# Kernel tuning notes

Hardware: AMD Instinct MI355X
Metric: run time of the kernel (lower is better)

## Reference

```python
import jax, jax.numpy as jnp
import numpy as np
from math import sqrt

H = 16  # head_num


def setup_inputs() -> dict:
    key = jax.random.key(0)
    ks = jax.random.split(key, 8)
    B, Sq, Skv, Dq, Dkv, Dall = 2, 2048, 2048, 1024, 1024, 1024
    x = jax.random.normal(ks[0], (B, Sq, Dq), dtype=jnp.float32)
    y = jax.random.normal(ks[1], (B, Skv, Dkv), dtype=jnp.float32)
    attention_mask = jnp.ones((B, 1, Sq, Skv), dtype=jnp.int32)
    # torch nn.Linear weights are [out, in]
    Wq = jax.random.normal(ks[2], (Dall, Dq), dtype=jnp.float32) * 0.02
    Wk = jax.random.normal(ks[3], (Dall, Dkv), dtype=jnp.float32) * 0.02
    Wv = jax.random.normal(ks[4], (Dall, Dkv), dtype=jnp.float32) * 0.02
    Wo = jax.random.normal(ks[5], (Dq, Dall), dtype=jnp.float32) * 0.02
    bo = jnp.zeros((Dq,), dtype=jnp.float32)
    return {"x": x, "y": y, "attention_mask": attention_mask,
            "Wq": Wq, "Wk": Wk, "Wv": Wv, "Wo": Wo, "bo": bo}


def reference(x, y, attention_mask, Wq, Wk, Wv, Wo, bo):
    B, Sq, _ = x.shape
    Dall = Wq.shape[0]
    Dh = Dall // H
    # projections (torch Linear: x @ W.T), split heads -> [B, H, S, Dh]
    q = (x @ Wq.T).reshape(B, Sq, H, Dh).transpose(0, 2, 1, 3)
    k = (y @ Wk.T).reshape(B, -1, H, Dh).transpose(0, 2, 1, 3)
    v = (y @ Wv.T).reshape(B, -1, H, Dh).transpose(0, 2, 1, 3)
    scores = jnp.einsum('bhqd,bhkd->bhqk', q, k)  # [B,H,Sq,Skv]
    mask = (attention_mask == 0)  # masked_fill where mask.eq(0) -> but torch does mask.eq(0) then fills True positions
    scores = jnp.where(mask, jnp.float32(-1e9), scores)
    # NOTE: faithful quirk - mask applied before scaling; scale uses sqrt(h_size)
    attn = jax.nn.softmax(scores / sqrt(Dh), axis=-1)
    out = jnp.einsum('bhqk,bhkd->bhqd', attn, v)
    out = out.transpose(0, 2, 1, 3).reshape(B, Sq, Dall)
    return out @ Wo.T + bo
```

## Files before the change

### kernel.cpp

```cpp
#include <hip/hip_runtime.h>
#include <stdint.h>


typedef __attribute__((ext_vector_type(8))) short bf16x8;
typedef __attribute__((ext_vector_type(4))) float f32x4;
typedef __attribute__((ext_vector_type(16))) float f32x16;
typedef __attribute__((ext_vector_type(2))) unsigned int u32x2;

#define LOG2E 1.44269504088896f
#define QSCALE (0.125f * LOG2E)

static __device__ __forceinline__ unsigned short f2bf(float f) {
  union { float f; unsigned int u; } v; v.f = f;
  unsigned int r = v.u + 0x7FFFu + ((v.u >> 16) & 1u);
  return (unsigned short)(r >> 16);
}

static __device__ __forceinline__ void g2l16(const void* gsrc, void* ldst) {
  __builtin_amdgcn_global_load_lds((const __attribute__((address_space(1))) unsigned int*)gsrc,
                                   (__attribute__((address_space(3))) unsigned int*)ldst,
                                   16, 0, 0);
}

static __device__ __forceinline__ unsigned int cvt_pk_bf16(float lo, float hi) {
  unsigned int r;
  asm("v_cvt_pk_bf16_f32 %0, %1, %2" : "=v"(r) : "v"(lo), "v"(hi));
  return r;
}

static __device__ __forceinline__ u32x2 pl32swap(unsigned int a, unsigned int b) {
  return __builtin_amdgcn_permlane32_swap(a, b, false, false);
}

static __device__ __forceinline__ f32x16 mfma32(bf16x8 a, bf16x8 b, f32x16 c) {
  return __builtin_amdgcn_mfma_f32_32x32x16_bf16(a, b, c, 0, 0, 0);
}

static __device__ __forceinline__ size_t kfrag_addr(int row, int col) {
  int b = row >> 11, s = row & 2047;
  int h = col >> 6, d = col & 63;
  int t32 = s >> 5, r31 = s & 31;
  int ks = d >> 4, r5 = (d >> 3) & 1, e = d & 7;
  return (size_t)(b * 16 + h) * 131072 + (size_t)t32 * 2048 + ks * 512 + (r5 * 32 + r31) * 8 + e;
}
static __device__ __forceinline__ size_t vfrag_addr(int row, int col) {
  int b = row >> 11, s = row & 2047;
  int h = col >> 6, d = col & 63;
  int t64 = s >> 6, k2 = (s >> 4) & 3, r5 = (s >> 3) & 1, e = s & 7;
  int mb = d >> 5, r31 = d & 31;
  return (size_t)(b * 16 + h) * 131072 + (size_t)t64 * 4096 + (mb * 4 + k2) * 512 + (r5 * 32 + r31) * 8 + e;
}

__global__ void k_prep(const float* __restrict__ x, const float* __restrict__ y,
                       const float* __restrict__ Wq, const float* __restrict__ Wk,
                       const float* __restrict__ Wv, const float* __restrict__ Wo,
                       const int* __restrict__ mask,
                       unsigned short* __restrict__ xb, unsigned short* __restrict__ yb,
                       unsigned short* __restrict__ Wqb, unsigned short* __restrict__ Wkb,
                       unsigned short* __restrict__ Wvb, unsigned short* __restrict__ Wob,
                       unsigned long long* __restrict__ bits, unsigned int* __restrict__ flag) {
  const int task = blockIdx.y;
  if (task == 6) {
    const int lane = threadIdx.x & 63;
    int gw = blockIdx.x * 4 + (threadIdx.x >> 6);
    bool any0 = false;
    for (; gw < 131072; gw += 4096) {
      int m = mask[(size_t)gw * 64 + lane];
      unsigned long long bal = __ballot(m != 0);
      if (lane == 0) {
        bits[gw] = bal;
        any0 |= (bal != ~0ull);
      }
    }
    if (lane == 0 && any0) atomicAnd(flag, 0u);
    return;
  }
  const float* in; unsigned short* out; int n;
  switch (task) {
    case 0: in = x;  out = xb;  n = 4194304; break;
    case 1: in = y;  out = yb;  n = 4194304; break;
    case 2: in = Wq; out = Wqb; n = 1048576; break;
    case 3: in = Wk; out = Wkb; n = 1048576; break;
    case 4: in = Wv; out = Wvb; n = 1048576; break;
    default: in = Wo; out = Wob; n = 1048576; break;
  }
  int i = (blockIdx.x * blockDim.x + threadIdx.x) * 4;
  const int stride = gridDim.x * blockDim.x * 4;
  for (; i < n; i += stride) {
    float4 v = *reinterpret_cast<const float4*>(in + i);
    ushort4 o;
    o.x = f2bf(v.x); o.y = f2bf(v.y); o.z = f2bf(v.z); o.w = f2bf(v.w);
    *reinterpret_cast<ushort4*>(out + i) = o;
  }
}

template <int OM>
static __device__ __forceinline__ void gemm_body(const unsigned short* __restrict__ A,
                                                 const unsigned short* __restrict__ W,
                                                 void* __restrict__ Cout,
                                                 float scale) {
  __shared__ __align__(16) unsigned short As[128 * 32];
  __shared__ __align__(16) unsigned short Bs[128 * 32];
  const int tid = threadIdx.x;
  const int w = tid >> 6, lane = tid & 63;
  const int wr = w >> 1, wc = w & 1;
  const int l15 = lane & 15, lg = lane >> 4;
  const int bm = blockIdx.x, bn = blockIdx.y;

  f32x4 acc[4][4] = {};

  const int e0 = w * 1024 + lane * 8;
  const int e1 = e0 + 512;
  const int r0 = e0 >> 5, c0 = e0 & 31;
  const int r1 = e1 >> 5, c1 = e1 & 31;
  const unsigned short* A0 = A + (size_t)(bm * 128 + r0) * 1024 + c0;
  const unsigned short* A1 = A + (size_t)(bm * 128 + r1) * 1024 + c1;
  const unsigned short* W0 = W + (size_t)(bn * 128 + r0) * 1024 + c0;
  const unsigned short* W1 = W + (size_t)(bn * 128 + r1) * 1024 + c1;

  for (int kt = 0; kt < 1024; kt += 32) {
    g2l16(A0 + kt, (char*)As + e0 * 2);
    g2l16(A1 + kt, (char*)As + e1 * 2);
    g2l16(W0 + kt, (char*)Bs + e0 * 2);
    g2l16(W1 + kt, (char*)Bs + e1 * 2);
    __syncthreads();
    bf16x8 a[4], b[4];
#pragma unroll
    for (int mi = 0; mi < 4; ++mi)
      a[mi] = *reinterpret_cast<const bf16x8*>(As + (wr * 64 + mi * 16 + l15) * 32 + lg * 8);
#pragma unroll
    for (int ni = 0; ni < 4; ++ni)
      b[ni] = *reinterpret_cast<const bf16x8*>(Bs + (wc * 64 + ni * 16 + l15) * 32 + lg * 8);
#pragma unroll
    for (int mi = 0; mi < 4; ++mi)
#pragma unroll
      for (int ni = 0; ni < 4; ++ni)
        acc[mi][ni] = __builtin_amdgcn_mfma_f32_16x16x32_bf16(a[mi], b[ni], acc[mi][ni], 0, 0, 0);
    __syncthreads();
  }

#pragma unroll
  for (int ni = 0; ni < 4; ++ni) {
    const int gcol = bn * 128 + wc * 64 + ni * 16 + l15;
#pragma unroll
    for (int mi = 0; mi < 4; ++mi) {
#pragma unroll
      for (int r = 0; r < 4; ++r) {
        const int grow = bm * 128 + wr * 64 + mi * 16 + lg * 4 + r;
        if (OM == 2)
          ((unsigned short*)Cout)[kfrag_addr(grow, gcol)] = f2bf(acc[mi][ni][r] * scale);
        else
          ((unsigned short*)Cout)[vfrag_addr(grow, gcol)] = f2bf(acc[mi][ni][r]);
      }
    }
  }
}

__global__ __launch_bounds__(256) void k_gemm_qkv(
    const unsigned short* __restrict__ xb, const unsigned short* __restrict__ yb,
    const unsigned short* __restrict__ Wq, const unsigned short* __restrict__ Wk,
    const unsigned short* __restrict__ Wv,
    unsigned short* __restrict__ Qf, unsigned short* __restrict__ Kf,
    unsigned short* __restrict__ Vf) {
  const int z = blockIdx.z;
  if (z == 0) gemm_body<2>(xb, Wq, Qf, QSCALE);
  else if (z == 1) gemm_body<2>(yb, Wk, Kf, 1.f);
  else gemm_body<3>(yb, Wv, Vf, 1.f);
}

__global__ __launch_bounds__(256) void k_gemm_o(
    const unsigned short* __restrict__ A, const unsigned short* __restrict__ W,
    float* __restrict__ out, const float* __restrict__ bo) {
  __shared__ __align__(16) unsigned short As[64 * 32];
  __shared__ __align__(16) unsigned short Bs[128 * 32];
  const int tid = threadIdx.x;
  const int w = tid >> 6, lane = tid & 63;
  const int l15 = lane & 15, lg = lane >> 4;
  const int bm = blockIdx.x, bn = blockIdx.y;

  f32x4 acc[4][2] = {};

  const int ea = tid * 8;
  const int eb0 = tid * 8;
  const int eb1 = eb0 + 2048;
  const int ra = ea >> 5, ca = ea & 31;
  const int rb0 = eb0 >> 5, cb0 = eb0 & 31;
  const int rb1 = eb1 >> 5, cb1 = eb1 & 31;
  const unsigned short* A0 = A + (size_t)(bm * 64 + ra) * 1024 + ca;
  const unsigned short* W0 = W + (size_t)(bn * 128 + rb0) * 1024 + cb0;
  const unsigned short* W1 = W + (size_t)(bn * 128 + rb1) * 1024 + cb1;

  for (int kt = 0; kt < 1024; kt += 32) {
    g2l16(A0 + kt, (char*)As + ea * 2);
    g2l16(W0 + kt, (char*)Bs + eb0 * 2);
    g2l16(W1 + kt, (char*)Bs + eb1 * 2);
    __syncthreads();
    bf16x8 a[4], b[2];
#pragma unroll
    for (int mi = 0; mi < 4; ++mi)
      a[mi] = *reinterpret_cast<const bf16x8*>(As + (mi * 16 + l15) * 32 + lg * 8);
#pragma unroll
    for (int ni = 0; ni < 2; ++ni)
      b[ni] = *reinterpret_cast<const bf16x8*>(Bs + (w * 32 + ni * 16 + l15) * 32 + lg * 8);
#pragma unroll
    for (int mi = 0; mi < 4; ++mi)
#pragma unroll
      for (int ni = 0; ni < 2; ++ni)
        acc[mi][ni] = __builtin_amdgcn_mfma_f32_16x16x32_bf16(a[mi], b[ni], acc[mi][ni], 0, 0, 0);
    __syncthreads();
  }

#pragma unroll
  for (int ni = 0; ni < 2; ++ni) {
    const int gcol = bn * 128 + w * 32 + ni * 16 + l15;
    const float bv = bo[gcol];
#pragma unroll
    for (int mi = 0; mi < 4; ++mi) {
#pragma unroll
      for (int r = 0; r < 4; ++r) {
        const int grow = bm * 64 + mi * 16 + lg * 4 + r;
        out[(size_t)grow * 1024 + gcol] = acc[mi][ni][r] + bv;
      }
    }
  }
}


#define BUILD_PB2(SP, K2, IDX) {                                   \
    unsigned int c0_ = cvt_pk_bf16(SP[(K2)*8 + 0], SP[(K2)*8 + 1]);\
    unsigned int c1_ = cvt_pk_bf16(SP[(K2)*8 + 2], SP[(K2)*8 + 3]);\
    unsigned int c2_ = cvt_pk_bf16(SP[(K2)*8 + 4], SP[(K2)*8 + 5]);\
    unsigned int c3_ = cvt_pk_bf16(SP[(K2)*8 + 6], SP[(K2)*8 + 7]);\
    u32x2 r0_ = pl32swap(c0_, c2_);                                \
    u32x2 r1_ = pl32swap(c1_, c3_);                                \
    union { unsigned int u[4]; bf16x8 v; } f_;                     \
    f_.u[0] = r0_.x; f_.u[1] = r1_.x; f_.u[2] = r0_.y; f_.u[3] = r1_.y; \
    pb[IDX] = f_.v; }

#define STAGE128(T, BUF) {                                                    \
    const char* ks_ = Kg + (size_t)(T) * 16384;                               \
    const char* vs_ = Vg + (size_t)(T) * 16384;                               \
    char* db_ = smem + (BUF) * 32768;                                         \
    const int lo_ = tid * 16;                                                 \
    _Pragma("unroll")                                                         \
    for (int c_ = 0; c_ < 4; ++c_) {                                          \
      g2l16(ks_ + c_ * 4096 + lo_, db_ + c_ * 4096 + lo_);                    \
      g2l16(vs_ + c_ * 4096 + lo_, db_ + 16384 + c_ * 4096 + lo_);            \
    }                                                                         \
  }

#define HALF_BODY(BASE, HALF, TW)                                             \
  {                                                                           \
    const char* Kb = (BASE) + (HALF) * 8192;                                  \
    const char* Vb = (BASE) + 16384 + (HALF) * 8192;                          \
    bf16x8 kf[8], vf[8];                                                      \
    _Pragma("unroll")                                                         \
    for (int f = 0; f < 8; ++f)                                               \
      kf[f] = *reinterpret_cast<const bf16x8*>(Kb + f * 1024 + lane * 16);    \
    f32x16 s0 = z16, s1 = z16;                                                \
    __builtin_amdgcn_s_setprio(1);                                            \
    _Pragma("unroll")                                                         \
    for (int ks = 0; ks < 4; ++ks) {                                          \
      s0 = mfma32(kf[ks], qf[ks], s0);                                        \
      s1 = mfma32(kf[4 + ks], qf[ks], s1);                                    \
    }                                                                         \
    __builtin_amdgcn_s_setprio(0);                                            \
    _Pragma("unroll")                                                         \
    for (int f = 0; f < 8; ++f)                                               \
      vf[f] = *reinterpret_cast<const bf16x8*>(Vb + f * 1024 + lane * 16);    \
    if (!allfull) {                                                           \
      unsigned long long wb = brow[TW];                                       \
      if (!__all(wb == ~0ull)) {                                              \
        _Pragma("unroll")                                                     \
        for (int r = 0; r < 16; ++r) {                                        \
          const int kl = (r & 3) + 8 * (r >> 2) + 4 * hi;                     \
          s0[r] = ((wb >> kl) & 1ull) ? s0[r] : -1e9f;                        \
          s1[r] = ((wb >> (kl + 32)) & 1ull) ? s1[r] : -1e9f;                 \
        }                                                                     \
      }                                                                       \
    }                                                                         \
    _Pragma("unroll")                                                         \
    for (int r = 0; r < 16; ++r) {                                            \
      s0[r] = __builtin_amdgcn_exp2f(s0[r]);                                  \
      s1[r] = __builtin_amdgcn_exp2f(s1[r]);                                  \
    }                                                                         \
    {                                                                         \
      float sm[8];                                                            \
      _Pragma("unroll")                                                       \
      for (int r = 0; r < 8; ++r) sm[r] = (s0[r] + s0[r + 8]) + (s1[r] + s1[r + 8]); \
      sm[0] += sm[4]; sm[1] += sm[5]; sm[2] += sm[6]; sm[3] += sm[7];         \
      sm[0] += sm[2]; sm[1] += sm[3];                                         \
      float ls = sm[0] + sm[1];                                               \
      u32x2 sw = pl32swap(__builtin_bit_cast(unsigned int, ls),               \
                          __builtin_bit_cast(unsigned int, ls));              \
      l_run += __builtin_bit_cast(float, sw.x) + __builtin_bit_cast(float, sw.y); \
    }                                                                         \
    bf16x8 pb[4];                                                             \
    BUILD_PB2(s0, 0, 0) BUILD_PB2(s0, 1, 1) BUILD_PB2(s1, 0, 2) BUILD_PB2(s1, 1, 3) \
    __builtin_amdgcn_s_setprio(1);                                            \
    _Pragma("unroll")                                                         \
    for (int k2 = 0; k2 < 4; ++k2) {                                          \
      o0 = mfma32(vf[k2], pb[k2], o0);                                        \
      o1 = mfma32(vf[4 + k2], pb[k2], o1);                                    \
    }                                                                         \
    __builtin_amdgcn_s_setprio(0);                                            \
  }

__global__ __launch_bounds__(256, 2) void k_attn(
    const unsigned short* __restrict__ Qf, const unsigned short* __restrict__ Kf,
    const unsigned short* __restrict__ Vf, const unsigned long long* __restrict__ bits,
    const unsigned int* __restrict__ flag, unsigned short* __restrict__ AO) {
  __shared__ __align__(16) char smem[65536];
  const int tid = threadIdx.x, w = tid >> 6, lane = tid & 63;
  const int l31 = lane & 31, hi = lane >> 5;
  const int bid = blockIdx.x;
  const int xcd = bid & 7, rr = bid >> 3;
  const int j = rr & 15;
  const int g = xcd + ((rr >> 4) << 3);
  const int h = g & 15, b = g >> 4;
  const int q = j * 128 + w * 32 + l31;
  const bool allfull = (*flag == 0xFFFFFFFFu);
  const f32x16 z16 = {};

  const size_t bh = (size_t)(b * 16 + h) * 131072;
  bf16x8 qf[4];
  const unsigned short* Qp = Qf + bh + (size_t)(j * 4 + w) * 2048 + lane * 8;
#pragma unroll
  for (int ks = 0; ks < 4; ++ks)
    qf[ks] = *reinterpret_cast<const bf16x8*>(Qp + ks * 512);

  const char* Kg = (const char*)(Kf + bh);
  const char* Vg = (const char*)(Vf + bh);
  const unsigned long long* brow = bits + (size_t)(b * 2048 + q) * 32;

  f32x16 o0 = {}, o1 = {};
  float l_run = 0.f;

  STAGE128(0, 0)
  __syncthreads();

  for (int t = 0; t < 16; ++t) {
    const int cur = t & 1;
    if (t < 15) STAGE128(t + 1, cur ^ 1)
    const char* base = smem + cur * 32768;
    HALF_BODY(base, 0, 2 * t)
    HALF_BODY(base, 1, 2 * t + 1)
    __syncthreads();
  }

  const float inv = 1.f / l_run;
  unsigned short* Orow = AO + (size_t)(b * 2048 + q) * 1024 + h * 64;
#pragma unroll
  for (int g2 = 0; g2 < 4; ++g2) {
    ushort4 pk;
    pk.x = f2bf(o0[g2 * 4 + 0] * inv);
    pk.y = f2bf(o0[g2 * 4 + 1] * inv);
    pk.z = f2bf(o0[g2 * 4 + 2] * inv);
    pk.w = f2bf(o0[g2 * 4 + 3] * inv);
    *reinterpret_cast<ushort4*>(Orow + 8 * g2 + 4 * hi) = pk;
    pk.x = f2bf(o1[g2 * 4 + 0] * inv);
    pk.y = f2bf(o1[g2 * 4 + 1] * inv);
    pk.z = f2bf(o1[g2 * 4 + 2] * inv);
    pk.w = f2bf(o1[g2 * 4 + 3] * inv);
    *reinterpret_cast<ushort4*>(Orow + 32 + 8 * g2 + 4 * hi) = pk;
  }
}

extern "C" void kernel_launch(void* const* d_in, const int* in_sizes, int n_in,
                              void* d_out, int out_size, void* d_ws, size_t ws_size,
                              hipStream_t stream) {
  const float* x  = (const float*)d_in[0];
  const float* y  = (const float*)d_in[1];
  const int* mask = (const int*)d_in[2];
  const float* Wq = (const float*)d_in[3];
  const float* Wk = (const float*)d_in[4];
  const float* Wv = (const float*)d_in[5];
  const float* Wo = (const float*)d_in[6];
  const float* bo = (const float*)d_in[7];

  char* ws = (char*)d_ws;
  const size_t MB = 1ull << 20;
  unsigned short* xb  = (unsigned short*)(ws + 0 * MB);
  unsigned short* yb  = (unsigned short*)(ws + 8 * MB);
  unsigned short* Wqb = (unsigned short*)(ws + 16 * MB);
  unsigned short* Wkb = (unsigned short*)(ws + 18 * MB);
  unsigned short* Wvb = (unsigned short*)(ws + 20 * MB);
  unsigned short* Wob = (unsigned short*)(ws + 22 * MB);
  unsigned short* Qf  = (unsigned short*)(ws + 24 * MB);
  unsigned short* Kf  = (unsigned short*)(ws + 32 * MB);
  unsigned short* Vf  = (unsigned short*)(ws + 40 * MB);
  unsigned short* AOb = (unsigned short*)(ws + 56 * MB);
  unsigned long long* bits = (unsigned long long*)(ws + 64 * MB);
  unsigned int* flag = (unsigned int*)(ws + 65 * MB);

  hipMemsetAsync(flag, 0xFF, 4, stream);
  k_prep<<<dim3(1024, 7), 256, 0, stream>>>(x, y, Wq, Wk, Wv, Wo, mask,
                                            xb, yb, Wqb, Wkb, Wvb, Wob, bits, flag);
  k_gemm_qkv<<<dim3(32, 8, 3), 256, 0, stream>>>(xb, yb, Wqb, Wkb, Wvb, Qf, Kf, Vf);
  k_attn<<<512, 256, 0, stream>>>(Qf, Kf, Vf, bits, flag, AOb);
  k_gemm_o<<<dim3(64, 8), 256, 0, stream>>>(AOb, Wob, (float*)d_out, bo);
}
```

Before: 129.4 us.

## Software-pipeline attention loop: overlap next tile QK^T with current softmax/PV

Restructures the attention main loop from 16 iterations of 128-key tiles (two halves each) into 32 iterations of 64-key tiles. Each step computes the QK^T MFMAs for the next tile while softmax and PV run on the previous tile's scores and V fragments held in registers. LDS use is halved to 32KB of double buffers, with a sync per 64-key tile. The goal is to overlap exp and VALU work with MFMA, at the cost of more live registers (two score sets and two V fragment sets) and twice as many barriers. The s_setprio hints are also removed.

```diff
diff --git a/kernel.cpp b/kernel.cpp
--- a/kernel.cpp
+++ b/kernel.cpp
@@ -237,57 +237,39 @@
     f_.u[0] = r0_.x; f_.u[1] = r1_.x; f_.u[2] = r0_.y; f_.u[3] = r1_.y; \
     pb[IDX] = f_.v; }
 
-#define STAGE128(T, BUF) {                                                    \
-    const char* ks_ = Kg + (size_t)(T) * 16384;                               \
-    const char* vs_ = Vg + (size_t)(T) * 16384;                               \
-    char* db_ = smem + (BUF) * 32768;                                         \
-    const int lo_ = tid * 16;                                                 \
-    _Pragma("unroll")                                                         \
-    for (int c_ = 0; c_ < 4; ++c_) {                                          \
-      g2l16(ks_ + c_ * 4096 + lo_, db_ + c_ * 4096 + lo_);                    \
-      g2l16(vs_ + c_ * 4096 + lo_, db_ + 16384 + c_ * 4096 + lo_);            \
-    }                                                                         \
-  }
-
-#define HALF_BODY(BASE, HALF, TW)                                             \
+#define STAGE_TILE(T, BUF) {                                                  \
+    const size_t toff_ = (size_t)(T) * 8192;                                  \
+    char* kb_ = smem + (BUF) * 16384;                                         \
+    const int o0_ = (w * 2 + 0) * 1024 + lane * 16;                           \
+    const int o1_ = (w * 2 + 1) * 1024 + lane * 16;                           \
+    g2l16(Kg + toff_ + o0_, kb_ + o0_);                                       \
+    g2l16(Kg + toff_ + o1_, kb_ + o1_);                                       \
+    g2l16(Vg + toff_ + o0_, kb_ + 8192 + o0_);                                \
+    g2l16(Vg + toff_ + o1_, kb_ + 8192 + o1_);                                \
+  }
+
+#define SM_PV(S0, S1, VF, T)                                                  \
   {                                                                           \
-    const char* Kb = (BASE) + (HALF) * 8192;                                  \
-    const char* Vb = (BASE) + 16384 + (HALF) * 8192;                          \
-    bf16x8 kf[8], vf[8];                                                      \
-    _Pragma("unroll")                                                         \
-    for (int f = 0; f < 8; ++f)                                               \
-      kf[f] = *reinterpret_cast<const bf16x8*>(Kb + f * 1024 + lane * 16);    \
-    f32x16 s0 = z16, s1 = z16;                                                \
-    __builtin_amdgcn_s_setprio(1);                                            \
-    _Pragma("unroll")                                                         \
-    for (int ks = 0; ks < 4; ++ks) {                                          \
-      s0 = mfma32(kf[ks], qf[ks], s0);                                        \
-      s1 = mfma32(kf[4 + ks], qf[ks], s1);                                    \
-    }                                                                         \
-    __builtin_amdgcn_s_setprio(0);                                            \
-    _Pragma("unroll")                                                         \
-    for (int f = 0; f < 8; ++f)                                               \
-      vf[f] = *reinterpret_cast<const bf16x8*>(Vb + f * 1024 + lane * 16);    \
     if (!allfull) {                                                           \
-      unsigned long long wb = brow[TW];                                       \
+      unsigned long long wb = brow[T];                                        \
       if (!__all(wb == ~0ull)) {                                              \
         _Pragma("unroll")                                                     \
         for (int r = 0; r < 16; ++r) {                                        \
           const int kl = (r & 3) + 8 * (r >> 2) + 4 * hi;                     \
-          s0[r] = ((wb >> kl) & 1ull) ? s0[r] : -1e9f;                        \
-          s1[r] = ((wb >> (kl + 32)) & 1ull) ? s1[r] : -1e9f;                 \
+          S0[r] = ((wb >> kl) & 1ull) ? S0[r] : -1e9f;                        \
+          S1[r] = ((wb >> (kl + 32)) & 1ull) ? S1[r] : -1e9f;                 \
         }                                                                     \
       }                                                                       \
     }                                                                         \
     _Pragma("unroll")                                                         \
     for (int r = 0; r < 16; ++r) {                                            \
-      s0[r] = __builtin_amdgcn_exp2f(s0[r]);                                  \
-      s1[r] = __builtin_amdgcn_exp2f(s1[r]);                                  \
+      S0[r] = __builtin_amdgcn_exp2f(S0[r]);                                  \
+      S1[r] = __builtin_amdgcn_exp2f(S1[r]);                                  \
     }                                                                         \
     {                                                                         \
       float sm[8];                                                            \
       _Pragma("unroll")                                                       \
-      for (int r = 0; r < 8; ++r) sm[r] = (s0[r] + s0[r + 8]) + (s1[r] + s1[r + 8]); \
+      for (int r = 0; r < 8; ++r) sm[r] = (S0[r] + S0[r + 8]) + (S1[r] + S1[r + 8]); \
       sm[0] += sm[4]; sm[1] += sm[5]; sm[2] += sm[6]; sm[3] += sm[7];         \
       sm[0] += sm[2]; sm[1] += sm[3];                                         \
       float ls = sm[0] + sm[1];                                               \
@@ -296,21 +278,40 @@
       l_run += __builtin_bit_cast(float, sw.x) + __builtin_bit_cast(float, sw.y); \
     }                                                                         \
     bf16x8 pb[4];                                                             \
-    BUILD_PB2(s0, 0, 0) BUILD_PB2(s0, 1, 1) BUILD_PB2(s1, 0, 2) BUILD_PB2(s1, 1, 3) \
-    __builtin_amdgcn_s_setprio(1);                                            \
+    BUILD_PB2(S0, 0, 0) BUILD_PB2(S0, 1, 1) BUILD_PB2(S1, 0, 2) BUILD_PB2(S1, 1, 3) \
     _Pragma("unroll")                                                         \
     for (int k2 = 0; k2 < 4; ++k2) {                                          \
-      o0 = mfma32(vf[k2], pb[k2], o0);                                        \
-      o1 = mfma32(vf[4 + k2], pb[k2], o1);                                    \
+      o0 = mfma32(VF[k2], pb[k2], o0);                                        \
+      o1 = mfma32(VF[4 + k2], pb[k2], o1);                                    \
     }                                                                         \
-    __builtin_amdgcn_s_setprio(0);                                            \
+  }
+
+#define PIPE_STEP(sO0, sO1, vfO, sN0, sN1, vfN, T)                            \
+  {                                                                           \
+    const char* base_ = smem + (((T) + 1) & 1) * 16384;                       \
+    bf16x8 kf[8];                                                             \
+    _Pragma("unroll")                                                         \
+    for (int f = 0; f < 8; ++f)                                               \
+      kf[f] = *reinterpret_cast<const bf16x8*>(base_ + f * 1024 + lane * 16); \
+    sN0 = z16; sN1 = z16;                                                     \
+    _Pragma("unroll")                                                         \
+    for (int ks = 0; ks < 4; ++ks) {                                          \
+      sN0 = mfma32(kf[ks], qf[ks], sN0);                                      \
+      sN1 = mfma32(kf[4 + ks], qf[ks], sN1);                                  \
+    }                                                                         \
+    SM_PV(sO0, sO1, vfO, T)                                                   \
+    _Pragma("unroll")                                                         \
+    for (int f = 0; f < 8; ++f)                                               \
+      vfN[f] = *reinterpret_cast<const bf16x8*>(base_ + 8192 + f * 1024 + lane * 16); \
+    if ((T) <= 29) STAGE_TILE((T) + 2, (T) & 1)                               \
+    __syncthreads();                                                          \
   }
 
 __global__ __launch_bounds__(256, 2) void k_attn(
     const unsigned short* __restrict__ Qf, const unsigned short* __restrict__ Kf,
     const unsigned short* __restrict__ Vf, const unsigned long long* __restrict__ bits,
     const unsigned int* __restrict__ flag, unsigned short* __restrict__ AO) {
-  __shared__ __align__(16) char smem[65536];
+  __shared__ __align__(16) char smem[32768];
   const int tid = threadIdx.x, w = tid >> 6, lane = tid & 63;
   const int l31 = lane & 31, hi = lane >> 5;
   const int bid = blockIdx.x;
@@ -336,17 +337,35 @@
   f32x16 o0 = {}, o1 = {};
   float l_run = 0.f;
 
-  STAGE128(0, 0)
+  f32x16 sA0, sA1, sB0, sB1;
+  bf16x8 vfA[8], vfB[8];
+
+  STAGE_TILE(0, 0)
   __syncthreads();
-
-  for (int t = 0; t < 16; ++t) {
-    const int cur = t & 1;
-    if (t < 15) STAGE128(t + 1, cur ^ 1)
-    const char* base = smem + cur * 32768;
-    HALF_BODY(base, 0, 2 * t)
-    HALF_BODY(base, 1, 2 * t + 1)
-    __syncthreads();
-  }
+  {
+    bf16x8 kf[8];
+#pragma unroll
+    for (int f = 0; f < 8; ++f)
+      kf[f] = *reinterpret_cast<const bf16x8*>(smem + f * 1024 + lane * 16);
+    sA0 = z16; sA1 = z16;
+#pragma unroll
+    for (int ks = 0; ks < 4; ++ks) {
+      sA0 = mfma32(kf[ks], qf[ks], sA0);
+      sA1 = mfma32(kf[4 + ks], qf[ks], sA1);
+    }
+#pragma unroll
+    for (int f = 0; f < 8; ++f)
+      vfA[f] = *reinterpret_cast<const bf16x8*>(smem + 8192 + f * 1024 + lane * 16);
+  }
+  STAGE_TILE(1, 1)
+  __syncthreads();
+
+  for (int tt = 0; tt < 30; tt += 2) {
+    PIPE_STEP(sA0, sA1, vfA, sB0, sB1, vfB, tt)
+    PIPE_STEP(sB0, sB1, vfB, sA0, sA1, vfA, tt + 1)
+  }
+  PIPE_STEP(sA0, sA1, vfA, sB0, sB1, vfB, 30)
+  SM_PV(sB0, sB1, vfB, 31)
 
   const float inv = 1.f / l_run;
   unsigned short* Orow = AO + (size_t)(b * 2048 + q) * 1024 + h * 64;
```

Result: no change. 129.2 us (-0.2%).
